# Kernel optimization log

Measured on AMD Instinct MI355X. Metric: run time of the kernel, lower is better.

Reference implementation:

```python
import jax, jax.numpy as jnp
import numpy as np

NUM_EXPERTS = 8
NUM_FEATURES = 2048


def setup_inputs() -> dict:
    key = jax.random.key(0)
    k1, k2, k3 = jax.random.split(key, 3)
    hidden_states = jax.random.normal(k1, (8192, NUM_FEATURES), dtype=jnp.float32)
    gate_up_proj = jax.random.normal(k2, (NUM_EXPERTS, NUM_FEATURES, 2 * NUM_FEATURES), dtype=jnp.float32)
    down_proj = jax.random.normal(k3, (NUM_EXPERTS, NUM_FEATURES, NUM_FEATURES), dtype=jnp.float32)
    return {"hidden_states": hidden_states, "gate_up_proj": gate_up_proj, "down_proj": down_proj}


def reference(hidden_states, gate_up_proj, down_proj):
    E, D = gate_up_proj.shape[0], gate_up_proj.shape[1]
    # (E, T, D) tokens pre-sorted per expert
    h = hidden_states.reshape(E, -1, D)
    # per-expert batched GEMM: (E, T, 2D)
    gate_up = jnp.einsum('etd,edf->etf', h, gate_up_proj)
    gate, up = gate_up[..., :D], gate_up[..., D:]
    # ReLU-gated activation, then down projection: (E, T, D)
    out = jnp.einsum('etd,edf->etf', up * jax.nn.relu(gate), down_proj)
    return out.reshape(-1, D)
```

## Files before the change

### kernel.cpp

```cpp
#include <hip/hip_runtime.h>
#include <stdint.h>


#define NEXP 8
#define DIM  2048
#define TOK  1024
#define NGU  4096
#define BM   128
#define BN   128
#define BK   32
#define LDST 40

typedef __attribute__((ext_vector_type(8))) short short8;
typedef __attribute__((ext_vector_type(4))) float f32x4;

__device__ __forceinline__ uint32_t pkbf(float lo, float hi) {
  return __builtin_amdgcn_perm(__float_as_uint(hi) + 0x8000u,
                               __float_as_uint(lo) + 0x8000u, 0x07060302u);
}

__device__ __forceinline__ uint16_t bf16_rne(float x) {
  uint32_t u = __float_as_uint(x);
  return (uint16_t)((u + 0x7fffu + ((u >> 16) & 1u)) >> 16);
}

__global__ __launch_bounds__(256, 2) void k_gateup(const float* __restrict__ H,
                                                   const float* __restrict__ W1,
                                                   uint16_t* __restrict__ ACT) {
  __shared__ uint16_t As[BM * LDST];
  __shared__ uint16_t Bg[BN * LDST];
  __shared__ uint16_t Bu[BN * LDST];

  const int tid = threadIdx.x;
  const int e   = blockIdx.z;
  const int m0  = blockIdx.y * BM;
  const int n0  = blockIdx.x * BN;

  const float* hA = H + (size_t)(e * TOK + m0) * DIM;
  const float* wE = W1 + (size_t)e * DIM * NGU;

  const int ar = tid >> 1;
  const int ak = (tid & 1) << 4;
  const float* aptr = hA + (size_t)ar * DIM + ak;
  uint16_t* asw = &As[ar * LDST + ak];

  const int bn = tid & 127;
  const int bk = (tid >> 7) << 4;
  const float* gptr = wE + (size_t)bk * NGU + (n0 + bn);
  const float* uptr = gptr + DIM;
  uint16_t* bgw = &Bg[bn * LDST + bk];
  uint16_t* buw = &Bu[bn * LDST + bk];

  const int lane = tid & 63;
  const int wid  = tid >> 6;
  const int wr = (wid >> 1) << 6;
  const int wc = (wid & 1) << 6;
  const int lm = lane & 15;
  const int qd = lane >> 4;

  f32x4 accg[4][4], accu[4][4];
  const f32x4 zero = {0.f, 0.f, 0.f, 0.f};
#pragma unroll
  for (int i = 0; i < 4; ++i)
#pragma unroll
    for (int j = 0; j < 4; ++j) { accg[i][j] = zero; accu[i][j] = zero; }

  const uint16_t* afr = &As[(wr + lm) * LDST + (qd << 3)];
  const uint16_t* gfr = &Bg[(wc + lm) * LDST + (qd << 3)];
  const uint16_t* ufr = &Bu[(wc + lm) * LDST + (qd << 3)];

  float4 a0 = *(const float4*)(aptr + 0);
  float4 a1 = *(const float4*)(aptr + 4);
  float4 a2 = *(const float4*)(aptr + 8);
  float4 a3 = *(const float4*)(aptr + 12);
  float g[16], u[16];
#pragma unroll
  for (int i = 0; i < 16; ++i) g[i] = gptr[(size_t)i * NGU];
#pragma unroll
  for (int i = 0; i < 16; ++i) u[i] = uptr[(size_t)i * NGU];

#pragma unroll 1
  for (int k0 = 0; k0 < DIM; k0 += BK) {
    uint4 aw0 = make_uint4(pkbf(a0.x, a0.y), pkbf(a0.z, a0.w),
                           pkbf(a1.x, a1.y), pkbf(a1.z, a1.w));
    uint4 aw1 = make_uint4(pkbf(a2.x, a2.y), pkbf(a2.z, a2.w),
                           pkbf(a3.x, a3.y), pkbf(a3.z, a3.w));
    uint4 gw0 = make_uint4(pkbf(g[0], g[1]),  pkbf(g[2], g[3]),
                           pkbf(g[4], g[5]),  pkbf(g[6], g[7]));
    uint4 gw1 = make_uint4(pkbf(g[8], g[9]),  pkbf(g[10], g[11]),
                           pkbf(g[12], g[13]), pkbf(g[14], g[15]));
    uint4 uw0 = make_uint4(pkbf(u[0], u[1]),  pkbf(u[2], u[3]),
                           pkbf(u[4], u[5]),  pkbf(u[6], u[7]));
    uint4 uw1 = make_uint4(pkbf(u[8], u[9]),  pkbf(u[10], u[11]),
                           pkbf(u[12], u[13]), pkbf(u[14], u[15]));

    __syncthreads();
    *(uint4*)(asw)     = aw0;
    *(uint4*)(asw + 8) = aw1;
    *(uint4*)(bgw)     = gw0;
    *(uint4*)(bgw + 8) = gw1;
    *(uint4*)(buw)     = uw0;
    *(uint4*)(buw + 8) = uw1;
    __syncthreads();

    aptr += BK;
    gptr += (size_t)BK * NGU;
    uptr += (size_t)BK * NGU;
    if (k0 + BK < DIM) {
      a0 = *(const float4*)(aptr + 0);
      a1 = *(const float4*)(aptr + 4);
      a2 = *(const float4*)(aptr + 8);
      a3 = *(const float4*)(aptr + 12);
#pragma unroll
      for (int i = 0; i < 16; ++i) g[i] = gptr[(size_t)i * NGU];
#pragma unroll
      for (int i = 0; i < 16; ++i) u[i] = uptr[(size_t)i * NGU];
    }

    short8 a[4], bgf[4], buf[4];
#pragma unroll
    for (int i = 0; i < 4; ++i) a[i] = *(const short8*)(afr + i * 16 * LDST);
#pragma unroll
    for (int j = 0; j < 4; ++j) {
      bgf[j] = *(const short8*)(gfr + j * 16 * LDST);
      buf[j] = *(const short8*)(ufr + j * 16 * LDST);
    }
#pragma unroll
    for (int i = 0; i < 4; ++i)
#pragma unroll
      for (int j = 0; j < 4; ++j) {
        accg[i][j] = __builtin_amdgcn_mfma_f32_16x16x32_bf16(a[i], bgf[j], accg[i][j], 0, 0, 0);
        accu[i][j] = __builtin_amdgcn_mfma_f32_16x16x32_bf16(a[i], buf[j], accu[i][j], 0, 0, 0);
      }
  }

  uint16_t* actE = ACT + (size_t)(e * TOK + m0) * DIM + n0;
#pragma unroll
  for (int i = 0; i < 4; ++i)
#pragma unroll
    for (int j = 0; j < 4; ++j)
#pragma unroll
      for (int t = 0; t < 4; ++t) {
        int row = wr + i * 16 + qd * 4 + t;
        int col = wc + j * 16 + lm;
        float gv = accg[i][j][t];
        float uv = accu[i][j][t];
        actE[(size_t)row * DIM + col] = bf16_rne(uv * fmaxf(gv, 0.f));
      }
}

__global__ __launch_bounds__(256, 2) void k_down(const uint16_t* __restrict__ ACT,
                                                 const float* __restrict__ W2,
                                                 float* __restrict__ OUT) {
  __shared__ uint16_t Bs[BN * LDST];

  const int tid = threadIdx.x;
  const int e   = blockIdx.z;
  const int m0  = blockIdx.y * BM;
  const int n0  = blockIdx.x * BN;

  const uint16_t* aA = ACT + (size_t)(e * TOK + m0) * DIM;
  const float* wE = W2 + (size_t)e * DIM * DIM;

  const int bn = tid & 127;
  const int bk = (tid >> 7) << 4;
  const float* bptr = wE + (size_t)bk * DIM + (n0 + bn);
  uint16_t* bsw = &Bs[bn * LDST + bk];

  const int lane = tid & 63;
  const int wid  = tid >> 6;
  const int wr = (wid >> 1) << 6;
  const int wc = (wid & 1) << 6;
  const int lm = lane & 15;
  const int qd = lane >> 4;

  const uint16_t* agp = aA + (size_t)(wr + lm) * DIM + (qd << 3);

  f32x4 acc[4][4];
  const f32x4 zero = {0.f, 0.f, 0.f, 0.f};
#pragma unroll
  for (int i = 0; i < 4; ++i)
#pragma unroll
    for (int j = 0; j < 4; ++j) acc[i][j] = zero;

  const uint16_t* bfr = &Bs[(wc + lm) * LDST + (qd << 3)];

  short8 an[4];
#pragma unroll
  for (int i = 0; i < 4; ++i) an[i] = *(const short8*)(agp + (size_t)i * 16 * DIM);
  float b[16];
#pragma unroll
  for (int i = 0; i < 16; ++i) b[i] = bptr[(size_t)i * DIM];

#pragma unroll 1
  for (int k0 = 0; k0 < DIM; k0 += BK) {
    uint4 bw0 = make_uint4(pkbf(b[0], b[1]),  pkbf(b[2], b[3]),
                           pkbf(b[4], b[5]),  pkbf(b[6], b[7]));
    uint4 bw1 = make_uint4(pkbf(b[8], b[9]),  pkbf(b[10], b[11]),
                           pkbf(b[12], b[13]), pkbf(b[14], b[15]));
    short8 a[4];
#pragma unroll
    for (int i = 0; i < 4; ++i) a[i] = an[i];

    __syncthreads();
    *(uint4*)(bsw)     = bw0;
    *(uint4*)(bsw + 8) = bw1;
    __syncthreads();

    bptr += (size_t)BK * DIM;
    agp  += BK;
    if (k0 + BK < DIM) {
#pragma unroll
      for (int i = 0; i < 4; ++i) an[i] = *(const short8*)(agp + (size_t)i * 16 * DIM);
#pragma unroll
      for (int i = 0; i < 16; ++i) b[i] = bptr[(size_t)i * DIM];
    }

    short8 bf[4];
#pragma unroll
    for (int j = 0; j < 4; ++j) bf[j] = *(const short8*)(bfr + j * 16 * LDST);
#pragma unroll
    for (int i = 0; i < 4; ++i)
#pragma unroll
      for (int j = 0; j < 4; ++j)
        acc[i][j] = __builtin_amdgcn_mfma_f32_16x16x32_bf16(a[i], bf[j], acc[i][j], 0, 0, 0);
  }

  float* outE = OUT + (size_t)(e * TOK + m0) * DIM + n0;
#pragma unroll
  for (int i = 0; i < 4; ++i)
#pragma unroll
    for (int j = 0; j < 4; ++j)
#pragma unroll
      for (int t = 0; t < 4; ++t) {
        int row = wr + i * 16 + qd * 4 + t;
        int col = wc + j * 16 + lm;
        outE[(size_t)row * DIM + col] = acc[i][j][t];
      }
}

extern "C" void kernel_launch(void* const* d_in, const int* in_sizes, int n_in,
                              void* d_out, int out_size, void* d_ws, size_t ws_size,
                              hipStream_t stream) {
  const float* H  = (const float*)d_in[0];
  const float* W1 = (const float*)d_in[1];
  const float* W2 = (const float*)d_in[2];
  float* OUT = (float*)d_out;
  uint16_t* ACT = (uint16_t*)d_ws;

  dim3 blk(256);
  dim3 g1(DIM / BN, TOK / BM, NEXP);
  k_gateup<<<g1, blk, 0, stream>>>(H, W1, ACT);
  dim3 g2(DIM / BN, TOK / BM, NEXP);
  k_down<<<g2, blk, 0, stream>>>(ACT, W2, OUT);
}
```

Measured before the change: 775.7 us.

## Pre-convert inputs to transposed bf16 and stream tiles via global_load_lds double buffering

Adds separate conversion kernels that turn hidden states into bf16 and weights into transposed bf16 copies in workspace. The GEMM kernels then load K-contiguous bf16 tiles straight into LDS with global_load_lds into two alternating buffers, removing per-iteration strided fp32 loads and in-register conversion. This costs extra full passes over weights (about 400MB read) every call plus workspace, and the unpadded LDS layout may cause bank conflicts. The old path is kept as a fallback when the workspace is too small.

```diff
diff --git a/kernel.cpp b/kernel.cpp
--- a/kernel.cpp
+++ b/kernel.cpp
@@ -19,14 +19,252 @@
                                __float_as_uint(lo) + 0x8000u, 0x07060302u);
 }
 
+__device__ __forceinline__ uint16_t bf16_rhu(float x) {
+  return (uint16_t)((__float_as_uint(x) + 0x8000u) >> 16);
+}
+
 __device__ __forceinline__ uint16_t bf16_rne(float x) {
   uint32_t u = __float_as_uint(x);
   return (uint16_t)((u + 0x7fffu + ((u >> 16) & 1u)) >> 16);
 }
 
-__global__ __launch_bounds__(256, 2) void k_gateup(const float* __restrict__ H,
-                                                   const float* __restrict__ W1,
-                                                   uint16_t* __restrict__ ACT) {
+__device__ __forceinline__ void gll16(const void* g, void* l) {
+  typedef __attribute__((address_space(1))) uint32_t gas_t;
+  typedef __attribute__((address_space(3))) uint32_t las_t;
+  __builtin_amdgcn_global_load_lds((gas_t*)(uintptr_t)g,
+                                   (las_t*)(uint32_t)(uintptr_t)l, 16, 0, 0);
+}
+
+
+__global__ __launch_bounds__(256) void k_cvt(const float* __restrict__ s,
+                                             uint16_t* __restrict__ d, int n8) {
+  for (int i = blockIdx.x * 256 + threadIdx.x; i < n8; i += gridDim.x * 256) {
+    const float4* p = (const float4*)(s + (size_t)i * 8);
+    float4 x = p[0], y = p[1];
+    *(uint4*)(d + (size_t)i * 8) =
+        make_uint4(pkbf(x.x, x.y), pkbf(x.z, x.w), pkbf(y.x, y.y), pkbf(y.z, y.w));
+  }
+}
+
+__global__ __launch_bounds__(256) void k_cvt_t(const float* __restrict__ src,
+                                               uint16_t* __restrict__ dst,
+                                               int K, int N) {
+  __shared__ uint16_t T[64][68];
+  const int e = blockIdx.z;
+  const int k0 = blockIdx.y << 6;
+  const int n0 = blockIdx.x << 6;
+  const float* s = src + (size_t)e * K * N;
+  uint16_t* d = dst + (size_t)e * N * K;
+  const int rr = threadIdx.x >> 4;
+  const int cc = (threadIdx.x & 15) << 2;
+#pragma unroll
+  for (int p = 0; p < 4; ++p) {
+    int kk = (p << 4) + rr;
+    float4 v = *(const float4*)(s + (size_t)(k0 + kk) * N + n0 + cc);
+    T[cc + 0][kk] = bf16_rhu(v.x);
+    T[cc + 1][kk] = bf16_rhu(v.y);
+    T[cc + 2][kk] = bf16_rhu(v.z);
+    T[cc + 3][kk] = bf16_rhu(v.w);
+  }
+  __syncthreads();
+#pragma unroll
+  for (int p = 0; p < 4; ++p) {
+    int nn = (p << 4) + rr;
+    *(ushort4*)(d + (size_t)(n0 + nn) * K + k0 + cc) =
+        make_ushort4(T[nn][cc], T[nn][cc + 1], T[nn][cc + 2], T[nn][cc + 3]);
+  }
+}
+
+
+__global__ __launch_bounds__(256, 2) void k_gateup_b(const uint16_t* __restrict__ Hb,
+                                                     const uint16_t* __restrict__ W1T,
+                                                     uint16_t* __restrict__ ACT) {
+  __shared__ uint16_t As[2][BM * BK];
+  __shared__ uint16_t Bg[2][BN * BK];
+  __shared__ uint16_t Bu[2][BN * BK];
+
+  const int tid = threadIdx.x;
+  const int e   = blockIdx.z;
+  const int m0  = blockIdx.y * BM;
+  const int n0  = blockIdx.x * BN;
+
+  const int sr = tid >> 2;
+  const int sk = (tid & 3) << 3;
+  const uint16_t* aG = Hb  + (size_t)(e * TOK + m0 + sr) * DIM + sk;
+  const uint16_t* gG = W1T + ((size_t)e * NGU + n0 + sr) * DIM + sk;
+  const uint16_t* uG = gG + (size_t)DIM * DIM;
+  const int l0 = tid * 8;
+  const int l1 = 2048 + tid * 8;
+  const size_t r1 = (size_t)64 * DIM;
+
+  const int lane = tid & 63;
+  const int wid  = tid >> 6;
+  const int wr = (wid >> 1) << 6;
+  const int wc = (wid & 1) << 6;
+  const int lm = lane & 15;
+  const int qd = lane >> 4;
+
+  f32x4 accg[4][4], accu[4][4];
+  const f32x4 zero = {0.f, 0.f, 0.f, 0.f};
+#pragma unroll
+  for (int i = 0; i < 4; ++i)
+#pragma unroll
+    for (int j = 0; j < 4; ++j) { accg[i][j] = zero; accu[i][j] = zero; }
+
+#define K1_STAGE(c, kk)                         \
+  do {                                          \
+    gll16(aG + (kk),      &As[c][l0]);          \
+    gll16(aG + (kk) + r1, &As[c][l1]);          \
+    gll16(gG + (kk),      &Bg[c][l0]);          \
+    gll16(gG + (kk) + r1, &Bg[c][l1]);          \
+    gll16(uG + (kk),      &Bu[c][l0]);          \
+    gll16(uG + (kk) + r1, &Bu[c][l1]);          \
+  } while (0)
+
+#define K1_COMPUTE(c)                                                          \
+  do {                                                                         \
+    const uint16_t* af = &As[c][(wr + lm) * BK + (qd << 3)];                   \
+    const uint16_t* gf = &Bg[c][(wc + lm) * BK + (qd << 3)];                   \
+    const uint16_t* uf = &Bu[c][(wc + lm) * BK + (qd << 3)];                   \
+    short8 a[4], bg[4], bu[4];                                                 \
+    _Pragma("unroll")                                                          \
+    for (int i = 0; i < 4; ++i) a[i] = *(const short8*)(af + i * 16 * BK);     \
+    _Pragma("unroll")                                                          \
+    for (int j = 0; j < 4; ++j) {                                              \
+      bg[j] = *(const short8*)(gf + j * 16 * BK);                              \
+      bu[j] = *(const short8*)(uf + j * 16 * BK);                              \
+    }                                                                          \
+    _Pragma("unroll")                                                          \
+    for (int i = 0; i < 4; ++i)                                                \
+      _Pragma("unroll")                                                        \
+      for (int j = 0; j < 4; ++j) {                                            \
+        accg[i][j] = __builtin_amdgcn_mfma_f32_16x16x32_bf16(a[i], bg[j],      \
+                                                             accg[i][j], 0, 0, 0); \
+        accu[i][j] = __builtin_amdgcn_mfma_f32_16x16x32_bf16(a[i], bu[j],      \
+                                                             accu[i][j], 0, 0, 0); \
+      }                                                                        \
+  } while (0)
+
+  K1_STAGE(0, 0);
+  __syncthreads();
+
+#pragma unroll 1
+  for (int k0 = 0; k0 < DIM; k0 += 2 * BK) {
+    if (k0 + BK < DIM) K1_STAGE(1, k0 + BK);
+    K1_COMPUTE(0);
+    __syncthreads();
+    if (k0 + 2 * BK < DIM) K1_STAGE(0, k0 + 2 * BK);
+    K1_COMPUTE(1);
+    __syncthreads();
+  }
+#undef K1_STAGE
+#undef K1_COMPUTE
+
+  uint16_t* actE = ACT + (size_t)(e * TOK + m0) * DIM + n0;
+#pragma unroll
+  for (int i = 0; i < 4; ++i)
+#pragma unroll
+    for (int j = 0; j < 4; ++j)
+#pragma unroll
+      for (int t = 0; t < 4; ++t) {
+        int row = wr + i * 16 + qd * 4 + t;
+        int col = wc + j * 16 + lm;
+        float gv = accg[i][j][t];
+        float uv = accu[i][j][t];
+        actE[(size_t)row * DIM + col] = bf16_rne(uv * fmaxf(gv, 0.f));
+      }
+}
+
+__global__ __launch_bounds__(256, 2) void k_down_b(const uint16_t* __restrict__ ACT,
+                                                   const uint16_t* __restrict__ W2T,
+                                                   float* __restrict__ OUT) {
+  __shared__ uint16_t As[2][BM * BK];
+  __shared__ uint16_t Bs[2][BN * BK];
+
+  const int tid = threadIdx.x;
+  const int e   = blockIdx.z;
+  const int m0  = blockIdx.y * BM;
+  const int n0  = blockIdx.x * BN;
+
+  const int sr = tid >> 2;
+  const int sk = (tid & 3) << 3;
+  const uint16_t* aG = ACT + (size_t)(e * TOK + m0 + sr) * DIM + sk;
+  const uint16_t* bG = W2T + ((size_t)e * DIM + n0 + sr) * DIM + sk;
+  const int l0 = tid * 8;
+  const int l1 = 2048 + tid * 8;
+  const size_t r1 = (size_t)64 * DIM;
+
+  const int lane = tid & 63;
+  const int wid  = tid >> 6;
+  const int wr = (wid >> 1) << 6;
+  const int wc = (wid & 1) << 6;
+  const int lm = lane & 15;
+  const int qd = lane >> 4;
+
+  f32x4 acc[4][4];
+  const f32x4 zero = {0.f, 0.f, 0.f, 0.f};
+#pragma unroll
+  for (int i = 0; i < 4; ++i)
+#pragma unroll
+    for (int j = 0; j < 4; ++j) acc[i][j] = zero;
+
+#define K2_STAGE(c, kk)                         \
+  do {                                          \
+    gll16(aG + (kk),      &As[c][l0]);          \
+    gll16(aG + (kk) + r1, &As[c][l1]);          \
+    gll16(bG + (kk),      &Bs[c][l0]);          \
+    gll16(bG + (kk) + r1, &Bs[c][l1]);          \
+  } while (0)
+
+#define K2_COMPUTE(c)                                                          \
+  do {                                                                         \
+    const uint16_t* af = &As[c][(wr + lm) * BK + (qd << 3)];                   \
+    const uint16_t* bf = &Bs[c][(wc + lm) * BK + (qd << 3)];                   \
+    short8 a[4], b[4];                                                         \
+    _Pragma("unroll")                                                          \
+    for (int i = 0; i < 4; ++i) a[i] = *(const short8*)(af + i * 16 * BK);     \
+    _Pragma("unroll")                                                          \
+    for (int j = 0; j < 4; ++j) b[j] = *(const short8*)(bf + j * 16 * BK);     \
+    _Pragma("unroll")                                                          \
+    for (int i = 0; i < 4; ++i)                                                \
+      _Pragma("unroll")                                                        \
+      for (int j = 0; j < 4; ++j)                                              \
+        acc[i][j] = __builtin_amdgcn_mfma_f32_16x16x32_bf16(a[i], b[j],        \
+                                                            acc[i][j], 0, 0, 0); \
+  } while (0)
+
+  K2_STAGE(0, 0);
+  __syncthreads();
+
+#pragma unroll 1
+  for (int k0 = 0; k0 < DIM; k0 += 2 * BK) {
+    if (k0 + BK < DIM) K2_STAGE(1, k0 + BK);
+    K2_COMPUTE(0);
+    __syncthreads();
+    if (k0 + 2 * BK < DIM) K2_STAGE(0, k0 + 2 * BK);
+    K2_COMPUTE(1);
+    __syncthreads();
+  }
+#undef K2_STAGE
+#undef K2_COMPUTE
+
+  float* outE = OUT + (size_t)(e * TOK + m0) * DIM + n0;
+#pragma unroll
+  for (int i = 0; i < 4; ++i)
+#pragma unroll
+    for (int j = 0; j < 4; ++j)
+#pragma unroll
+      for (int t = 0; t < 4; ++t) {
+        int row = wr + i * 16 + qd * 4 + t;
+        int col = wc + j * 16 + lm;
+        outE[(size_t)row * DIM + col] = acc[i][j][t];
+      }
+}
+
+
+__global__ __launch_bounds__(256, 2) void k_gateup_fb(const float* __restrict__ H,
+                                                      const float* __restrict__ W1,
+                                                      uint16_t* __restrict__ ACT) {
   __shared__ uint16_t As[BM * LDST];
   __shared__ uint16_t Bg[BN * LDST];
   __shared__ uint16_t Bu[BN * LDST];
@@ -149,9 +387,9 @@
       }
 }
 
-__global__ __launch_bounds__(256, 2) void k_down(const uint16_t* __restrict__ ACT,
-                                                 const float* __restrict__ W2,
-                                                 float* __restrict__ OUT) {
+__global__ __launch_bounds__(256, 2) void k_down_fb(const uint16_t* __restrict__ ACT,
+                                                    const float* __restrict__ W2,
+                                                    float* __restrict__ OUT) {
   __shared__ uint16_t Bs[BN * LDST];
 
   const int tid = threadIdx.x;
@@ -239,6 +477,7 @@
       }
 }
 
+
 extern "C" void kernel_launch(void* const* d_in, const int* in_sizes, int n_in,
                               void* d_out, int out_size, void* d_ws, size_t ws_size,
                               hipStream_t stream) {
@@ -246,11 +485,29 @@
   const float* W1 = (const float*)d_in[1];
   const float* W2 = (const float*)d_in[2];
   float* OUT = (float*)d_out;
-  uint16_t* ACT = (uint16_t*)d_ws;
+
+  const size_t ACT_B = (size_t)NEXP * TOK * DIM * 2;
+  const size_t HB_B  = (size_t)NEXP * TOK * DIM * 2;
+  const size_t W1T_B = (size_t)NEXP * DIM * NGU * 2;
+  const size_t W2T_B = (size_t)NEXP * DIM * DIM * 2;
 
   dim3 blk(256);
-  dim3 g1(DIM / BN, TOK / BM, NEXP);
-  k_gateup<<<g1, blk, 0, stream>>>(H, W1, ACT);
-  dim3 g2(DIM / BN, TOK / BM, NEXP);
-  k_down<<<g2, blk, 0, stream>>>(ACT, W2, OUT);
-}
+  dim3 gg(DIM / BN, TOK / BM, NEXP);
+
+  if (ws_size >= ACT_B + HB_B + W1T_B + W2T_B) {
+    uint16_t* ACT = (uint16_t*)d_ws;
+    uint16_t* Hb  = (uint16_t*)((char*)d_ws + ACT_B);
+    uint16_t* W1T = (uint16_t*)((char*)d_ws + ACT_B + HB_B);
+    uint16_t* W2T = (uint16_t*)((char*)d_ws + ACT_B + HB_B + W1T_B);
+
+    k_cvt<<<2048, blk, 0, stream>>>(H, Hb, NEXP * TOK * DIM / 8);
+    k_cvt_t<<<dim3(NGU / 64, DIM / 64, NEXP), blk, 0, stream>>>(W1, W1T, DIM, NGU);
+    k_cvt_t<<<dim3(DIM / 64, DIM / 64, NEXP), blk, 0, stream>>>(W2, W2T, DIM, DIM);
+    k_gateup_b<<<gg, blk, 0, stream>>>(Hb, W1T, ACT);
+    k_down_b<<<gg, blk, 0, stream>>>(ACT, W2T, OUT);
+  } else {
+    uint16_t* ACT = (uint16_t*)d_ws;
+    k_gateup_fb<<<gg, blk, 0, stream>>>(H, W1, ACT);
+    k_down_fb<<<gg, blk, 0, stream>>>(ACT, W2, OUT);
+  }
+}
```

Result: faster. 747.0 us (-3.7%).
